# Kernel tuning notes

Hardware: AMD Instinct MI355X
Metric: run time of the kernel (lower is better)

The kernel has to match this reference:

```python
import jax, jax.numpy as jnp
import numpy as np
from jax import lax

EPS = 1e-12  # torch F.normalize eps

def conv2d(x, w, padding, groups=1):
    return lax.conv_general_dilated(
        x, w, window_strides=(1, 1), padding=padding,
        dimension_numbers=('NCHW', 'OIHW', 'NCHW'),
        feature_group_count=groups)

def setup_inputs() -> dict:
    key = jax.random.key(0)
    ks = jax.random.split(key, 6)
    B, C, H, W = 4, 192, 192, 192
    heads = 6
    s = 0.02
    return {
        'x': jax.random.normal(ks[0], (B, C, H, W), jnp.float32),
        'y': jax.random.normal(ks[1], (B, C, H, W), jnp.float32),
        'q_w': jax.random.normal(ks[2], (C, C, 3, 3), jnp.float32) * s,
        'kv_w': jax.random.normal(ks[3], (2 * C, C, 1, 1), jnp.float32) * s,
        'kvdw_w': jax.random.normal(ks[4], (2 * C, 1, 3, 3), jnp.float32) * s,
        'proj_w': jax.random.normal(ks[5], (C, C, 1, 1), jnp.float32) * s,
        'temperature': jnp.ones((heads, 1, 1), jnp.float32),
        'num_heads': heads,
    }

def reference(x, y, q_w, kv_w, kvdw_w, proj_w, temperature, num_heads):
    b, c, h, w = x.shape
    # kv path: 1x1 conv then 3x3 depthwise conv (groups = 2c)
    kv = conv2d(y, kv_w, 'VALID')
    kv = conv2d(kv, kvdw_w, 'SAME', groups=2 * c)
    k, v = jnp.split(kv, 2, axis=1)
    # q path: 3x3 conv
    q = conv2d(x, q_w, 'SAME')
    # b (head c) h w -> b head c (h w)
    def to_heads(t):
        return t.reshape(b, num_heads, c // num_heads, h * w)
    q, k, v = to_heads(q), to_heads(k), to_heads(v)
    # L2-normalize over spatial (hw) dim
    q = q / jnp.maximum(jnp.linalg.norm(q, axis=-1, keepdims=True), EPS)
    k = k / jnp.maximum(jnp.linalg.norm(k, axis=-1, keepdims=True), EPS)
    # channel attention: [b, head, c, c]
    attn = jnp.einsum('bhcn,bhdn->bhcd', q, k) * temperature
    attn = jax.nn.softmax(attn, axis=-1)
    out = jnp.einsum('bhcd,bhdn->bhcn', attn, v)
    out = out.reshape(b, c, h, w)
    out = conv2d(out, proj_w, 'VALID')
    return out
```

## Files before the change

### kernel.cpp

```cpp
#include <hip/hip_runtime.h>


#define DEV static __device__ __forceinline__

typedef __attribute__((ext_vector_type(8))) unsigned short U16x8;
typedef __attribute__((ext_vector_type(4))) unsigned short U16x4;
typedef __attribute__((ext_vector_type(8))) __bf16 BF16x8;
typedef __attribute__((ext_vector_type(4))) float F32x4;

DEV unsigned short f2bf(float f) {
  unsigned u = __float_as_uint(f);
  u += 0x7FFFu + ((u >> 16) & 1u);
  return (unsigned short)(u >> 16);
}
DEV float bf2f(unsigned short h) { return __uint_as_float(((unsigned)h) << 16); }

#define NB 4
#define NC 192
#define NHW 36864
#define IMG 7077888

__global__ void k_detect(const void* temp_in, int* flag, float* temp6) {
  if (threadIdx.x == 0) {
    unsigned bits = *(const unsigned*)temp_in;
    int isbf = ((bits & 0xFFFFu) == 0x3F80u) ? 1 : 0;
    *flag = isbf;
    for (int h = 0; h < 6; ++h) {
      float t = isbf ? bf2f(((const unsigned short*)temp_in)[h])
                     : ((const float*)temp_in)[h];
      temp6[h] = t;
    }
  }
}

__global__ void k_prep(const void* qw, const void* kvw, const void* pjw, const void* dww,
                       const int* flagp, unsigned short* wt9, unsigned short* kvwt,
                       unsigned short* pjwt, float* dwt) {
  int flag = *flagp;
  for (int i = blockIdx.x * 256 + threadIdx.x; i < 445824; i += gridDim.x * 256) {
    if (i < 331776) {
      int tap = i / 36864, r = i - tap * 36864;
      int src = r * 9 + tap;
      float v = flag ? bf2f(((const unsigned short*)qw)[src]) : ((const float*)qw)[src];
      wt9[i] = f2bf(v);
    } else if (i < 405504) {
      int j = i - 331776;
      float v = flag ? bf2f(((const unsigned short*)kvw)[j]) : ((const float*)kvw)[j];
      kvwt[j] = f2bf(v);
    } else if (i < 442368) {
      int j = i - 405504;
      float v = flag ? bf2f(((const unsigned short*)pjw)[j]) : ((const float*)pjw)[j];
      pjwt[j] = f2bf(v);
    } else {
      int j = i - 442368;
      int c = j / 9, tap = j - c * 9;
      float v = flag ? bf2f(((const unsigned short*)dww)[j]) : ((const float*)dww)[j];
      dwt[tap * 384 + c] = v;
    }
  }
}

__global__ __launch_bounds__(256) void k_transpose(const void* xin, const void* yin,
                                                   const int* flagp,
                                                   unsigned short* xt, unsigned short* yt) {
  __shared__ unsigned short tile[32][65];
  int flag = *flagp;
  const void* src = blockIdx.z ? yin : xin;
  unsigned short* dst = blockIdx.z ? yt : xt;
  int n0 = blockIdx.x * 64;
  int b = blockIdx.y / 6, c0 = (blockIdx.y % 6) * 32;
  size_t base_in = (size_t)b * IMG;
  int tid = threadIdx.x;
  int nl = tid & 63, cl0 = tid >> 6;
  for (int i = 0; i < 8; ++i) {
    int cl = cl0 + i * 4;
    size_t idx = base_in + (size_t)(c0 + cl) * NHW + n0 + nl;
    unsigned short v = flag ? ((const unsigned short*)src)[idx]
                            : f2bf(((const float*)src)[idx]);
    tile[cl][nl] = v;
  }
  __syncthreads();
  int nl2 = tid >> 2, co = (tid & 3) * 8;
  U16x8 v;
  #pragma unroll
  for (int j = 0; j < 8; ++j) v[j] = tile[co + j][nl2];
  *(U16x8*)(dst + (size_t)b * IMG + (size_t)(n0 + nl2) * NC + c0 + co) = v;
}

__global__ __launch_bounds__(256) void k_conv1x1(const unsigned short* yt,
                                                 const unsigned short* kvwt,
                                                 unsigned short* kv0) {
  __shared__ unsigned short As[192 * 40];
  __shared__ unsigned short Bs[64 * 40];
  int b = blockIdx.z, octile = blockIdx.y, n0 = blockIdx.x * 64;
  const unsigned short* ybase = yt + (size_t)b * IMG;
  int tid = threadIdx.x, wave = tid >> 6, lane = tid & 63;
  int quad = lane >> 4, m = lane & 15;
  F32x4 acc[3][4] = {};
  for (int kc = 0; kc < 6; ++kc) {
    int k0 = kc * 32;
    for (int u = tid; u < 768; u += 256) {
      int row = u >> 2, oct = u & 3;
      U16x8 v = *(const U16x8*)(kvwt + (size_t)(octile * 192 + row) * 192 + k0 + oct * 8);
      *(U16x8*)(As + row * 40 + oct * 8) = v;
    }
    {
      int row = tid >> 2, oct = tid & 3;
      U16x8 v = *(const U16x8*)(ybase + (size_t)(n0 + row) * NC + k0 + oct * 8);
      *(U16x8*)(Bs + row * 40 + oct * 8) = v;
    }
    __syncthreads();
    BF16x8 bfr[4];
    #pragma unroll
    for (int cf = 0; cf < 4; ++cf)
      bfr[cf] = *(const BF16x8*)(Bs + (cf * 16 + m) * 40 + quad * 8);
    #pragma unroll
    for (int rf = 0; rf < 3; ++rf) {
      BF16x8 afr = *(const BF16x8*)(As + (wave * 48 + rf * 16 + m) * 40 + quad * 8);
      #pragma unroll
      for (int cf = 0; cf < 4; ++cf)
        acc[rf][cf] = __builtin_amdgcn_mfma_f32_16x16x32_bf16(afr, bfr[cf], acc[rf][cf], 0, 0, 0);
    }
    __syncthreads();
  }
  #pragma unroll
  for (int rf = 0; rf < 3; ++rf)
    #pragma unroll
    for (int cf = 0; cf < 4; ++cf) {
      int nl = cf * 16 + m;
      int oc = octile * 192 + wave * 48 + rf * 16 + quad * 4;
      U16x4 s;
      #pragma unroll
      for (int r = 0; r < 4; ++r) s[r] = f2bf(acc[rf][cf][r]);
      *(U16x4*)(kv0 + (size_t)b * 14155776 + (size_t)(n0 + nl) * 384 + oc) = s;
    }
}

__global__ __launch_bounds__(256) void k_dw(const unsigned short* kv0, const float* dwt,
                                            unsigned short* knchw, unsigned short* vnhwc) {
  __shared__ unsigned short lt[96 * 72];
  int b = blockIdx.z, cg = blockIdx.y, t = blockIdx.x;
  int h = t / 3, w0 = (t % 3) * 64;
  int c0 = cg * 96;
  const unsigned short* kb = kv0 + (size_t)b * 14155776;
  int tid = threadIdx.x;
  for (int u = tid; u < 768; u += 256) {
    int wl = u / 12, cv = u - wl * 12;
    int cc = c0 + cv * 8;
    float r[8] = {0.f, 0.f, 0.f, 0.f, 0.f, 0.f, 0.f, 0.f};
    for (int dy = 0; dy < 3; ++dy) {
      int sr = h + dy - 1;
      if (sr < 0 || sr >= 192) continue;
      for (int dx = 0; dx < 3; ++dx) {
        int sw = w0 + wl + dx - 1;
        if (sw < 0 || sw >= 192) continue;
        int tap = dy * 3 + dx;
        U16x8 v = *(const U16x8*)(kb + (size_t)(sr * 192 + sw) * 384 + cc);
        const float* dptr = dwt + tap * 384 + cc;
        #pragma unroll
        for (int j = 0; j < 8; ++j) r[j] += bf2f(v[j]) * dptr[j];
      }
    }
    if (cg < 2) {
      #pragma unroll
      for (int j = 0; j < 8; ++j) lt[(cv * 8 + j) * 72 + wl] = f2bf(r[j]);
    } else {
      U16x8 s;
      #pragma unroll
      for (int j = 0; j < 8; ++j) s[j] = f2bf(r[j]);
      *(U16x8*)(vnhwc + (size_t)b * IMG + (size_t)(h * 192 + w0 + wl) * NC + (cc - 192)) = s;
    }
  }
  if (cg < 2) {
    __syncthreads();
    for (int u = tid; u < 768; u += 256) {
      int cl = u >> 3, wo = u & 7;
      U16x8 s = *(const U16x8*)(lt + cl * 72 + wo * 8);
      *(U16x8*)(knchw + (size_t)b * IMG + (size_t)(c0 + cl) * NHW + h * 192 + w0 + wo * 8) = s;
    }
  }
}

__global__ __launch_bounds__(256) void k_conv3x3(const unsigned short* xt,
                                                 const unsigned short* wt9,
                                                 unsigned short* q) {
  __shared__ unsigned short As[128 * 40];
  __shared__ unsigned short Bs[192 * 40];
  int b = blockIdx.y, nt = blockIdx.x;
  int n0 = nt * 128;
  const unsigned short* xb = xt + (size_t)b * IMG;
  int tid = threadIdx.x, wave = tid >> 6, lane = tid & 63;
  int quad = lane >> 4, m = lane & 15;
  F32x4 acc[8][3] = {};
  for (int tap = 0; tap < 9; ++tap) {
    int dy = tap / 3, dx = tap - dy * 3;
    for (int kc = 0; kc < 6; ++kc) {
      int k0 = kc * 32;
      for (int u = tid; u < 512; u += 256) {
        int rl = u >> 2, oct = u & 3;
        int n = n0 + rl;
        int hh = n / 192, wr = n - hh * 192;
        int sr = hh + dy - 1, sw = wr + dx - 1;
        U16x8 v = {};
        if (sr >= 0 && sr < 192 && sw >= 0 && sw < 192)
          v = *(const U16x8*)(xb + (size_t)(sr * 192 + sw) * NC + k0 + oct * 8);
        *(U16x8*)(As + rl * 40 + oct * 8) = v;
      }
      for (int u = tid; u < 768; u += 256) {
        int row = u >> 2, oct = u & 3;
        U16x8 v = *(const U16x8*)(wt9 + (size_t)tap * 36864 + row * 192 + k0 + oct * 8);
        *(U16x8*)(Bs + row * 40 + oct * 8) = v;
      }
      __syncthreads();
      BF16x8 afr[8];
      #pragma unroll
      for (int rf = 0; rf < 8; ++rf)
        afr[rf] = *(const BF16x8*)(As + (rf * 16 + m) * 40 + quad * 8);
      #pragma unroll
      for (int cf = 0; cf < 3; ++cf) {
        BF16x8 bfr = *(const BF16x8*)(Bs + (wave * 48 + cf * 16 + m) * 40 + quad * 8);
        #pragma unroll
        for (int rf = 0; rf < 8; ++rf)
          acc[rf][cf] = __builtin_amdgcn_mfma_f32_16x16x32_bf16(afr[rf], bfr, acc[rf][cf], 0, 0, 0);
      }
      __syncthreads();
    }
  }
  size_t qb = (size_t)b * IMG;
  #pragma unroll
  for (int rf = 0; rf < 8; ++rf)
    #pragma unroll
    for (int cf = 0; cf < 3; ++cf) {
      int oc = wave * 48 + cf * 16 + m;
      int nl = rf * 16 + quad * 4;
      U16x4 s;
      #pragma unroll
      for (int r = 0; r < 4; ++r) s[r] = f2bf(acc[rf][cf][r]);
      *(U16x4*)(q + qb + (size_t)oc * NHW + n0 + nl) = s;
    }
}

__global__ __launch_bounds__(256) void k_gram(const unsigned short* q,
                                              const unsigned short* k, float* G) {
  __shared__ unsigned short Zs[64 * 72];
  int b = blockIdx.z, h = blockIdx.y, sp = blockIdx.x;
  const unsigned short* qb = q + (size_t)b * IMG + (size_t)h * 32 * NHW;
  const unsigned short* kb = k + (size_t)b * IMG + (size_t)h * 32 * NHW;
  int tid = threadIdx.x, wave = tid >> 6, lane = tid & 63;
  int quad = lane >> 4, m = lane & 15;
  F32x4 acc[4] = {};
  for (int it = 0; it < 18; ++it) {
    int nb = sp * 1152 + it * 64;
    for (int u = tid; u < 512; u += 256) {
      int row = u >> 3, oct = u & 7;
      const unsigned short* src = (row < 32) ? (qb + (size_t)row * NHW)
                                             : (kb + (size_t)(row - 32) * NHW);
      U16x8 v = *(const U16x8*)(src + nb + oct * 8);
      *(U16x8*)(Zs + row * 72 + oct * 8) = v;
    }
    __syncthreads();
    #pragma unroll
    for (int ks = 0; ks < 2; ++ks) {
      BF16x8 afr = *(const BF16x8*)(Zs + (wave * 16 + m) * 72 + ks * 32 + quad * 8);
      #pragma unroll
      for (int cg = 0; cg < 4; ++cg) {
        BF16x8 bfr = *(const BF16x8*)(Zs + (cg * 16 + m) * 72 + ks * 32 + quad * 8);
        acc[cg] = __builtin_amdgcn_mfma_f32_16x16x32_bf16(afr, bfr, acc[cg], 0, 0, 0);
      }
    }
    __syncthreads();
  }
  float* Gb = G + (size_t)(b * 6 + h) * 4096;
  #pragma unroll
  for (int cg = 0; cg < 4; ++cg) {
    int s = cg * 16 + m;
    #pragma unroll
    for (int r = 0; r < 4; ++r) {
      int row = wave * 16 + quad * 4 + r;
      atomicAdd(Gb + row * 64 + s, acc[cg][r]);
    }
  }
}

__global__ __launch_bounds__(256) void k_attn(const float* G, const float* temp6,
                                              const unsigned short* pjw,
                                              unsigned short* M) {
  __shared__ float attn[32][33];
  int bh = blockIdx.x;
  int b = bh / 6, h = bh - b * 6;
  const float* Gb = G + (size_t)bh * 4096;
  int tid = threadIdx.x;
  float temp = temp6[h];
  if (tid < 32) {
    int c = tid;
    float qn = sqrtf(fmaxf(Gb[c * 64 + c], 0.f));
    qn = fmaxf(qn, 1e-12f);
    float s[32];
    float mx = -1e30f;
    for (int d = 0; d < 32; ++d) {
      float kn = sqrtf(fmaxf(Gb[(32 + d) * 64 + 32 + d], 0.f));
      kn = fmaxf(kn, 1e-12f);
      float v = Gb[c * 64 + 32 + d] / (qn * kn) * temp;
      s[d] = v;
      mx = fmaxf(mx, v);
    }
    float sum = 0.f;
    for (int d = 0; d < 32; ++d) { float e = __expf(s[d] - mx); s[d] = e; sum += e; }
    float inv = 1.f / sum;
    for (int d = 0; d < 32; ++d) attn[c][d] = s[d] * inv;
  }
  __syncthreads();
  for (int u = tid; u < 6144; u += 256) {
    int oc = u >> 5, d = u & 31;
    float sum = 0.f;
    #pragma unroll
    for (int c = 0; c < 32; ++c)
      sum += bf2f(pjw[oc * 192 + h * 32 + c]) * attn[c][d];
    M[(size_t)b * 36864 + oc * 192 + h * 32 + d] = f2bf(sum);
  }
}

__global__ __launch_bounds__(256) void k_out(const unsigned short* v,
                                             const unsigned short* M,
                                             const int* flagp, void* out) {
  __shared__ unsigned short As[64 * 40];
  __shared__ unsigned short Bs[192 * 40];
  int b = blockIdx.y, nt = blockIdx.x;
  int n0 = nt * 64;
  const unsigned short* vb = v + (size_t)b * IMG;
  const unsigned short* Mb = M + (size_t)b * 36864;
  int tid = threadIdx.x, wave = tid >> 6, lane = tid & 63;
  int quad = lane >> 4, m = lane & 15;
  F32x4 acc[4][3] = {};
  for (int kc = 0; kc < 6; ++kc) {
    int k0 = kc * 32;
    {
      int rl = tid >> 2, oct = tid & 3;
      U16x8 vv = *(const U16x8*)(vb + (size_t)(n0 + rl) * NC + k0 + oct * 8);
      *(U16x8*)(As + rl * 40 + oct * 8) = vv;
    }
    for (int u = tid; u < 768; u += 256) {
      int row = u >> 2, oct = u & 3;
      U16x8 vv = *(const U16x8*)(Mb + row * 192 + k0 + oct * 8);
      *(U16x8*)(Bs + row * 40 + oct * 8) = vv;
    }
    __syncthreads();
    BF16x8 afr[4];
    #pragma unroll
    for (int rf = 0; rf < 4; ++rf)
      afr[rf] = *(const BF16x8*)(As + (rf * 16 + m) * 40 + quad * 8);
    #pragma unroll
    for (int cf = 0; cf < 3; ++cf) {
      BF16x8 bfr = *(const BF16x8*)(Bs + (wave * 48 + cf * 16 + m) * 40 + quad * 8);
      #pragma unroll
      for (int rf = 0; rf < 4; ++rf)
        acc[rf][cf] = __builtin_amdgcn_mfma_f32_16x16x32_bf16(afr[rf], bfr, acc[rf][cf], 0, 0, 0);
    }
    __syncthreads();
  }
  int flag = *flagp;
  #pragma unroll
  for (int rf = 0; rf < 4; ++rf)
    #pragma unroll
    for (int cf = 0; cf < 3; ++cf) {
      int oc = wave * 48 + cf * 16 + m;
      int nl = rf * 16 + quad * 4;
      size_t off = (size_t)b * IMG + (size_t)oc * NHW + n0 + nl;
      if (flag) {
        U16x4 s;
        #pragma unroll
        for (int r = 0; r < 4; ++r) s[r] = f2bf(acc[rf][cf][r]);
        *(U16x4*)((unsigned short*)out + off) = s;
      } else {
        F32x4 s;
        #pragma unroll
        for (int r = 0; r < 4; ++r) s[r] = acc[rf][cf][r];
        *(F32x4*)((float*)out + off) = s;
      }
    }
}

extern "C" void kernel_launch(void* const* d_in, const int* in_sizes, int n_in,
                              void* d_out, int out_size, void* d_ws, size_t ws_size,
                              hipStream_t stream) {
  (void)in_sizes; (void)n_in; (void)out_size; (void)ws_size;
  char* p = (char*)d_ws;
  int*            flag  = (int*)p;
  float*          temp6 = (float*)(p + 16);
  unsigned short* wt9   = (unsigned short*)(p + 256);
  unsigned short* kvwt  = (unsigned short*)(p + 663808);
  float*          dwt   = (float*)(p + 811264);
  unsigned short* pjwt  = (unsigned short*)(p + 825088);
  unsigned short* xt    = (unsigned short*)(p + 1048576);
  unsigned short* yt    = (unsigned short*)(p + 57671680);
  unsigned short* kv0   = (unsigned short*)(p + 114294784);
  unsigned short* vv    = (unsigned short*)(p + 227540992);
  float*          G     = (float*)(p + 284164096);
  unsigned short* M     = (unsigned short*)(p + 284557312);
  unsigned short* kq    = yt;
  unsigned short* q     = kv0;

  hipMemsetAsync(G, 0, (size_t)24 * 4096 * 4, stream);
  k_detect<<<1, 64, 0, stream>>>(d_in[6], flag, temp6);
  k_prep<<<512, 256, 0, stream>>>(d_in[2], d_in[3], d_in[5], d_in[4],
                                  flag, wt9, kvwt, pjwt, dwt);
  k_transpose<<<dim3(576, 24, 2), 256, 0, stream>>>(d_in[0], d_in[1], flag, xt, yt);
  k_conv1x1<<<dim3(576, 2, 4), 256, 0, stream>>>(yt, kvwt, kv0);
  k_dw<<<dim3(576, 4, 4), 256, 0, stream>>>(kv0, dwt, kq, vv);
  k_conv3x3<<<dim3(288, 4), 256, 0, stream>>>(xt, wt9, q);
  k_gram<<<dim3(32, 6, 4), 256, 0, stream>>>(q, kq, G);
  k_attn<<<24, 256, 0, stream>>>(G, temp6, pjwt, M);
  k_out<<<dim3(576, 4), 256, 0, stream>>>(vv, M, flag, d_out);
}
```

Before: 845.8 us.

## Pad x with zero halo and use direct global-to-LDS loads in 3x3 conv

The transpose now writes x into a zero-padded 194x194 NHWC buffer, with a small kernel clearing the halo, so the 3x3 conv no longer needs bounds checks. The conv loads A and B tiles with global_load_lds, using 64-wide K chunks and an XOR-swizzled LDS layout in place of padded rows, which removes register staging and cuts the number of barriers. G and M now reuse the padded buffer's memory, so their memset is moved after the conv. There is still no double buffering, so load latency is exposed at each barrier.

```diff
diff --git a/kernel.cpp b/kernel.cpp
--- a/kernel.cpp
+++ b/kernel.cpp
@@ -15,10 +15,17 @@
 }
 DEV float bf2f(unsigned short h) { return __uint_as_float(((unsigned)h) << 16); }
 
-#define NB 4
+DEV void gl2lds16(const unsigned short* g, void* l) {
+  __builtin_amdgcn_global_load_lds(
+      (const __attribute__((address_space(1))) unsigned int*)g,
+      (__attribute__((address_space(3))) unsigned int*)l, 16, 0, 0);
+}
+
 #define NC 192
 #define NHW 36864
 #define IMG 7077888
+#define PP 194
+#define PIMG 7226112
 
 __global__ void k_detect(const void* temp_in, int* flag, float* temp6) {
   if (threadIdx.x == 0) {
@@ -60,13 +67,26 @@
   }
 }
 
+__global__ void k_halo(unsigned short* xpad) {
+  unsigned short* p = xpad + (size_t)blockIdx.x * PIMG;
+  U16x8 z = {};
+  for (int i = threadIdx.x; i < 4656; i += 256) {
+    *(U16x8*)(p + i * 8) = z;
+    *(U16x8*)(p + (size_t)193 * PP * 192 + i * 8) = z;
+  }
+  for (int u = threadIdx.x; u < 4608; u += 256) {
+    int ph = 1 + u / 24, vj = u % 24;
+    *(U16x8*)(p + ((size_t)ph * PP) * 192 + vj * 8) = z;
+    *(U16x8*)(p + ((size_t)ph * PP + 193) * 192 + vj * 8) = z;
+  }
+}
+
 __global__ __launch_bounds__(256) void k_transpose(const void* xin, const void* yin,
                                                    const int* flagp,
-                                                   unsigned short* xt, unsigned short* yt) {
+                                                   unsigned short* xpad, unsigned short* yt) {
   __shared__ unsigned short tile[32][65];
   int flag = *flagp;
   const void* src = blockIdx.z ? yin : xin;
-  unsigned short* dst = blockIdx.z ? yt : xt;
   int n0 = blockIdx.x * 64;
   int b = blockIdx.y / 6, c0 = (blockIdx.y % 6) * 32;
   size_t base_in = (size_t)b * IMG;
@@ -84,7 +104,13 @@
   U16x8 v;
   #pragma unroll
   for (int j = 0; j < 8; ++j) v[j] = tile[co + j][nl2];
-  *(U16x8*)(dst + (size_t)b * IMG + (size_t)(n0 + nl2) * NC + c0 + co) = v;
+  int n = n0 + nl2;
+  if (blockIdx.z == 0) {
+    int hh = n / 192, ww = n - hh * 192;
+    *(U16x8*)(xpad + (size_t)b * PIMG + ((size_t)(hh + 1) * PP + (ww + 1)) * 192 + c0 + co) = v;
+  } else {
+    *(U16x8*)(yt + (size_t)b * IMG + (size_t)n * NC + c0 + co) = v;
+  }
 }
 
 __global__ __launch_bounds__(256) void k_conv1x1(const unsigned short* yt,
@@ -181,47 +207,61 @@
   }
 }
 
-__global__ __launch_bounds__(256) void k_conv3x3(const unsigned short* xt,
+__global__ __launch_bounds__(256) void k_conv3x3(const unsigned short* xpad,
                                                  const unsigned short* wt9,
                                                  unsigned short* q) {
-  __shared__ unsigned short As[128 * 40];
-  __shared__ unsigned short Bs[192 * 40];
+  __shared__ unsigned short As[8192];
+  __shared__ unsigned short Bs[12288];
   int b = blockIdx.y, nt = blockIdx.x;
   int n0 = nt * 128;
-  const unsigned short* xb = xt + (size_t)b * IMG;
+  const unsigned short* xb = xpad + (size_t)b * PIMG;
   int tid = threadIdx.x, wave = tid >> 6, lane = tid & 63;
   int quad = lane >> 4, m = lane & 15;
+  int ocs = (lane & 7) ^ ((lane >> 3) & 7);
+  int aoff[4];
+  #pragma unroll
+  for (int j = 0; j < 4; ++j) {
+    int row = (wave * 4 + j) * 8 + (lane >> 3);
+    int n = n0 + row;
+    int hh = n / 192, ww = n - hh * 192;
+    aoff[j] = (hh * PP + ww) * 192 + ocs * 8;
+  }
+  int boff[6];
+  #pragma unroll
+  for (int j = 0; j < 6; ++j) {
+    int row = (wave * 6 + j) * 8 + (lane >> 3);
+    boff[j] = row * 192 + ocs * 8;
+  }
+  int xa0 = ((quad) ^ (m & 7)) * 16;
+  int xa1 = ((4 + quad) ^ (m & 7)) * 16;
   F32x4 acc[8][3] = {};
   for (int tap = 0; tap < 9; ++tap) {
     int dy = tap / 3, dx = tap - dy * 3;
-    for (int kc = 0; kc < 6; ++kc) {
-      int k0 = kc * 32;
-      for (int u = tid; u < 512; u += 256) {
-        int rl = u >> 2, oct = u & 3;
-        int n = n0 + rl;
-        int hh = n / 192, wr = n - hh * 192;
-        int sr = hh + dy - 1, sw = wr + dx - 1;
-        U16x8 v = {};
-        if (sr >= 0 && sr < 192 && sw >= 0 && sw < 192)
-          v = *(const U16x8*)(xb + (size_t)(sr * 192 + sw) * NC + k0 + oct * 8);
-        *(U16x8*)(As + rl * 40 + oct * 8) = v;
-      }
-      for (int u = tid; u < 768; u += 256) {
-        int row = u >> 2, oct = u & 3;
-        U16x8 v = *(const U16x8*)(wt9 + (size_t)tap * 36864 + row * 192 + k0 + oct * 8);
-        *(U16x8*)(Bs + row * 40 + oct * 8) = v;
-      }
+    int tapo = (dy * PP + dx) * 192;
+    const unsigned short* wtb = wt9 + tap * 36864;
+    for (int kc = 0; kc < 3; ++kc) {
+      int ko = kc * 64;
+      #pragma unroll
+      for (int j = 0; j < 4; ++j)
+        gl2lds16(xb + aoff[j] + tapo + ko, (char*)As + (wave * 4 + j) * 1024);
+      #pragma unroll
+      for (int j = 0; j < 6; ++j)
+        gl2lds16(wtb + boff[j] + ko, (char*)Bs + (wave * 6 + j) * 1024);
       __syncthreads();
-      BF16x8 afr[8];
-      #pragma unroll
-      for (int rf = 0; rf < 8; ++rf)
-        afr[rf] = *(const BF16x8*)(As + (rf * 16 + m) * 40 + quad * 8);
-      #pragma unroll
-      for (int cf = 0; cf < 3; ++cf) {
-        BF16x8 bfr = *(const BF16x8*)(Bs + (wave * 48 + cf * 16 + m) * 40 + quad * 8);
+      #pragma unroll
+      for (int ks = 0; ks < 2; ++ks) {
+        int xa = ks ? xa1 : xa0;
+        BF16x8 afr[8];
         #pragma unroll
         for (int rf = 0; rf < 8; ++rf)
-          acc[rf][cf] = __builtin_amdgcn_mfma_f32_16x16x32_bf16(afr[rf], bfr, acc[rf][cf], 0, 0, 0);
+          afr[rf] = *(const BF16x8*)((const char*)As + (rf * 16 + m) * 128 + xa);
+        #pragma unroll
+        for (int cf = 0; cf < 3; ++cf) {
+          BF16x8 bfr = *(const BF16x8*)((const char*)Bs + (wave * 48 + cf * 16 + m) * 128 + xa);
+          #pragma unroll
+          for (int rf = 0; rf < 8; ++rf)
+            acc[rf][cf] = __builtin_amdgcn_mfma_f32_16x16x32_bf16(afr[rf], bfr, acc[rf][cf], 0, 0, 0);
+        }
       }
       __syncthreads();
     }
@@ -387,27 +427,28 @@
   char* p = (char*)d_ws;
   int*            flag  = (int*)p;
   float*          temp6 = (float*)(p + 16);
-  unsigned short* wt9   = (unsigned short*)(p + 256);
-  unsigned short* kvwt  = (unsigned short*)(p + 663808);
-  float*          dwt   = (float*)(p + 811264);
-  unsigned short* pjwt  = (unsigned short*)(p + 825088);
-  unsigned short* xt    = (unsigned short*)(p + 1048576);
-  unsigned short* yt    = (unsigned short*)(p + 57671680);
-  unsigned short* kv0   = (unsigned short*)(p + 114294784);
-  unsigned short* vv    = (unsigned short*)(p + 227540992);
-  float*          G     = (float*)(p + 284164096);
-  unsigned short* M     = (unsigned short*)(p + 284557312);
+  unsigned short* wt9   = (unsigned short*)(p + 64);
+  unsigned short* kvwt  = (unsigned short*)(p + 663616);
+  float*          dwt   = (float*)(p + 811072);
+  unsigned short* pjwt  = (unsigned short*)(p + 824896);
+  unsigned short* xpad  = (unsigned short*)(p + 898624);
+  unsigned short* yt    = (unsigned short*)(p + 58707520);
+  unsigned short* kv0   = (unsigned short*)(p + 115330624);
+  unsigned short* vv    = (unsigned short*)(p + 228576832);
+  float*          G     = (float*)xpad;
+  unsigned short* M     = (unsigned short*)((char*)xpad + 393216);
   unsigned short* kq    = yt;
   unsigned short* q     = kv0;
 
-  hipMemsetAsync(G, 0, (size_t)24 * 4096 * 4, stream);
   k_detect<<<1, 64, 0, stream>>>(d_in[6], flag, temp6);
   k_prep<<<512, 256, 0, stream>>>(d_in[2], d_in[3], d_in[5], d_in[4],
                                   flag, wt9, kvwt, pjwt, dwt);
-  k_transpose<<<dim3(576, 24, 2), 256, 0, stream>>>(d_in[0], d_in[1], flag, xt, yt);
+  k_halo<<<4, 256, 0, stream>>>(xpad);
+  k_transpose<<<dim3(576, 24, 2), 256, 0, stream>>>(d_in[0], d_in[1], flag, xpad, yt);
   k_conv1x1<<<dim3(576, 2, 4), 256, 0, stream>>>(yt, kvwt, kv0);
   k_dw<<<dim3(576, 4, 4), 256, 0, stream>>>(kv0, dwt, kq, vv);
-  k_conv3x3<<<dim3(288, 4), 256, 0, stream>>>(xt, wt9, q);
+  k_conv3x3<<<dim3(288, 4), 256, 0, stream>>>(xpad, wt9, q);
+  hipMemsetAsync(G, 0, (size_t)24 * 4096 * 4, stream);
   k_gram<<<dim3(32, 6, 4), 256, 0, stream>>>(q, kq, G);
   k_attn<<<24, 256, 0, stream>>>(G, temp6, pjwt, M);
   k_out<<<dim3(576, 4), 256, 0, stream>>>(vv, M, flag, d_out);
```

Result: faster. 729.9 us (-13.7%).
